# Performance work log

Measured on AMD Instinct MI355X. Metric: run time of the kernel, lower is better.

## Reference

```python
import jax, jax.numpy as jnp
import numpy as np

D_MODEL, N_HEADS, D_C, D_COMP, D_ROPE = 2048, 16, 512, 768, 64
D_HEAD = D_MODEL // N_HEADS  # 128
B, S = 2, 2048
ROPE_THETA = 10000.0


def _rope_cos_sin(seq_len, dim):
    # frequencies for pairwise complex rotation, dim = per-head rope dim (even)
    inv_freq = 1.0 / (ROPE_THETA ** (jnp.arange(0, dim, 2, dtype=jnp.float32) / dim))
    t = jnp.arange(seq_len, dtype=jnp.float32)
    ang = t[:, None] * inv_freq[None, :]  # [S, dim/2]
    return jnp.cos(ang), jnp.sin(ang)


def _apply_rope(x, cos, sin):
    # x: [B, S, H, dr]; rotate consecutive pairs (view_as_complex semantics)
    x1, x2 = x[..., 0::2], x[..., 1::2]
    c = cos[None, :, None, :]
    s = sin[None, :, None, :]
    y1 = x1 * c - x2 * s
    y2 = x1 * s + x2 * c
    return jnp.stack([y1, y2], axis=-1).reshape(x.shape)


def setup_inputs() -> dict:
    key = jax.random.key(0)
    ks = jax.random.split(key, 9)
    sc = 0.02
    return {
        "x": jax.random.normal(ks[0], (B, S, D_MODEL), jnp.float32),
        "Wd": jax.random.normal(ks[1], (D_MODEL, D_C), jnp.float32) * sc,
        "bd": jnp.zeros((D_C,), jnp.float32),
        "Wu": jax.random.normal(ks[2], (D_C, N_HEADS * D_HEAD), jnp.float32) * sc,
        "bu": jnp.zeros((N_HEADS * D_HEAD,), jnp.float32),
        "Wqd": jax.random.normal(ks[3], (D_MODEL, D_COMP), jnp.float32) * sc,
        "bqd": jnp.zeros((D_COMP,), jnp.float32),
        "Wqu": jax.random.normal(ks[4], (D_COMP, N_HEADS * D_HEAD), jnp.float32) * sc,
        "bqu": jnp.zeros((N_HEADS * D_HEAD,), jnp.float32),
        "Wqr": jax.random.normal(ks[5], (D_COMP, N_HEADS * D_ROPE), jnp.float32) * sc,
        "bqr": jnp.zeros((N_HEADS * D_ROPE,), jnp.float32),
        "Wkr": jax.random.normal(ks[6], (D_MODEL, N_HEADS * D_ROPE), jnp.float32) * sc,
        "bkr": jnp.zeros((N_HEADS * D_ROPE,), jnp.float32),
        "Wo": jax.random.normal(ks[7], (N_HEADS * D_HEAD, D_MODEL), jnp.float32) * sc,
        "bo": jnp.zeros((D_MODEL,), jnp.float32),
    }


def reference(x, Wd, bd, Wu, bu, Wqd, bqd, Wqu, bqu, Wqr, bqr, Wkr, bkr, Wo, bo):
    b, s, _ = x.shape
    # low-rank KV compression
    kv_c = x @ Wd + bd                                   # [B,S,d_c]
    kv_up = (kv_c @ Wu + bu).reshape(b, s, N_HEADS, D_HEAD)  # shared K-content / V
    # low-rank Q compression
    q_cmp = x @ Wqd + bqd                                # [B,S,d_comp]
    q_c = (q_cmp @ Wqu + bqu).reshape(b, s, N_HEADS, D_HEAD)
    # decoupled RoPE branches
    cos, sin = _rope_cos_sin(s, D_ROPE)
    q_r = _apply_rope((q_cmp @ Wqr + bqr).reshape(b, s, N_HEADS, D_ROPE), cos, sin)
    k_r = _apply_rope((x @ Wkr + bkr).reshape(b, s, N_HEADS, D_ROPE), cos, sin)
    q = jnp.concatenate([q_c, q_r], axis=-1)             # [B,S,H,dh+dr]
    k = jnp.concatenate([kv_up, k_r], axis=-1)           # [B,S,H,dh+dr]
    scale = 1.0 / np.sqrt(D_HEAD).astype(np.float32)
    scores = jnp.einsum('bqhd,bkhd->bhqk', q, k) * scale  # [B,H,S,S]
    probs = jax.nn.softmax(scores, axis=-1)
    out = jnp.einsum('bhqk,bkhd->bqhd', probs, kv_up)    # v == kv_up (as in source)
    out = out.reshape(b, s, N_HEADS * D_HEAD)
    return out @ Wo + bo
```

## Files before the change

kernel.cpp:

```cpp
#include <hip/hip_runtime.h>
#include <cmath>

typedef __bf16 bf16;
typedef __bf16 bf16x8 __attribute__((ext_vector_type(8)));
typedef __bf16 bf16x4 __attribute__((ext_vector_type(4)));
typedef __bf16 bf16x2 __attribute__((ext_vector_type(2)));
typedef float f32x4 __attribute__((ext_vector_type(4)));
typedef int i32x4 __attribute__((ext_vector_type(4)));

#define S_LEN 2048
#define QK_LD 3072

__device__ __forceinline__ void async_copy16(const bf16* g, bf16* l) {
    __builtin_amdgcn_global_load_lds(
        (const __attribute__((address_space(1))) void*)g,
        (__attribute__((address_space(3))) void*)l, 16, 0, 0);
}

__device__ __forceinline__ unsigned packbf(float a, float b) {
    bf16x2 v; v[0] = (bf16)a; v[1] = (bf16)b;
    return __builtin_bit_cast(unsigned, v);
}

__global__ __launch_bounds__(256) void cast_f32_bf16(const float* __restrict__ in,
                                                     bf16* __restrict__ out) {
    size_t i = ((size_t)blockIdx.x * 256 + threadIdx.x) * 8;
    float4 a = *(const float4*)(in + i);
    float4 b = *(const float4*)(in + i + 4);
    bf16x8 v;
    v[0] = (bf16)a.x; v[1] = (bf16)a.y; v[2] = (bf16)a.z; v[3] = (bf16)a.w;
    v[4] = (bf16)b.x; v[5] = (bf16)b.y; v[6] = (bf16)b.z; v[7] = (bf16)b.w;
    *(bf16x8*)(out + i) = v;
}

struct TSeg { const float* src; bf16* dst; int K, N, blk0; };
struct TArgs { TSeg s[7]; };

__global__ __launch_bounds__(256) void transpose_all(TArgs a) {
    __shared__ float tile[64][68];
    int b = blockIdx.x, si = 0;
#pragma unroll
    for (int i = 1; i < 7; ++i) if (b >= a.s[i].blk0) si = i;
    TSeg sg = a.s[si];
    int local = b - sg.blk0;
    int kTiles = sg.K >> 6;
    int kt = local % kTiles, nt = local / kTiles;
    int k0 = kt * 64, n0 = nt * 64;
    int K = sg.K, N = sg.N;
    int t = threadIdx.x;
#pragma unroll
    for (int i = 0; i < 4; ++i) {
        int c = t + i * 256;
        int r = c >> 4, off = (c & 15) * 4;
        float4 v = *(const float4*)(sg.src + (size_t)(k0 + r) * N + n0 + off);
        tile[r][off] = v.x; tile[r][off + 1] = v.y;
        tile[r][off + 2] = v.z; tile[r][off + 3] = v.w;
    }
    __syncthreads();
#pragma unroll
    for (int i = 0; i < 2; ++i) {
        int c = t + i * 256;
        int nr = c >> 3, koff = (c & 7) * 8;
        bf16x8 v;
#pragma unroll
        for (int j = 0; j < 8; ++j) v[j] = (bf16)tile[koff + j][nr];
        *(bf16x8*)(sg.dst + (size_t)(n0 + nr) * K + k0 + koff) = v;
    }
}

__global__ __launch_bounds__(256) void setup_small(const float* __restrict__ bd,
                                                   const float* __restrict__ bqd,
                                                   const float* __restrict__ bkr,
                                                   const float* __restrict__ bqu,
                                                   const float* __restrict__ bqr,
                                                   float* __restrict__ bcat,
                                                   float2* __restrict__ tab) {
    if (blockIdx.x < 21) {
        int i = blockIdx.x * 256 + threadIdx.x;
        if (i < 512) bcat[i] = bd[i];
        else if (i < 1280) bcat[i] = bqd[i - 512];
        else if (i < 2304) bcat[i] = bkr[i - 1280];
        else if (i < 4352) bcat[i] = bqu[i - 2304];
        else if (i < 5376) bcat[i] = bqr[i - 4352];
    } else {
        int id = (blockIdx.x - 21) * 256 + threadIdx.x;
        int s = id >> 5, i = id & 31;
        float f = expf(-0.2878231366242557f * (float)i);
        float ang = (float)s * f;
        tab[id] = make_float2(cosf(ang), sinf(ang));
    }
}

__device__ __forceinline__ void gemm_core(const bf16* __restrict__ A, int lda,
                                          const bf16* __restrict__ Bt,
                                          const float* __restrict__ bias,
                                          void* __restrict__ out0,
                                          void* __restrict__ out1,
                                          int Ndim, int Kdim, int mode,
                                          const float2* __restrict__ tab,
                                          int bn, int bm, bf16* As, bf16* Bs) {
    int t = threadIdx.x;
    int w = t >> 6, lane = t & 63;
    int wm = (w >> 1) * 64, wn = (w & 1) * 64;
    int l15 = lane & 15, q4 = lane >> 4;
    f32x4 acc[4][4] = {};

    int lrow = lane >> 2;
    int lcol = (lane & 3) * 8;
    int c0 = w * 2, c1 = w * 2 + 1;
    const bf16* aS0 = A  + (size_t)(bm * 128 + c0 * 16 + lrow) * lda + lcol;
    const bf16* aS1 = A  + (size_t)(bm * 128 + c1 * 16 + lrow) * lda + lcol;
    const bf16* bS0 = Bt + (size_t)(bn * 128 + c0 * 16 + lrow) * Kdim + lcol;
    const bf16* bS1 = Bt + (size_t)(bn * 128 + c1 * 16 + lrow) * Kdim + lcol;
    bf16* aD0 = &As[c0 * 512]; bf16* aD1 = &As[c1 * 512];
    bf16* bD0 = &Bs[c0 * 512]; bf16* bD1 = &Bs[c1 * 512];

    for (int kt = 0; kt < Kdim; kt += 32) {
        async_copy16(aS0 + kt, aD0);
        async_copy16(aS1 + kt, aD1);
        async_copy16(bS0 + kt, bD0);
        async_copy16(bS1 + kt, bD1);
        __syncthreads();
        bf16x8 af[4], bfr[4];
#pragma unroll
        for (int mb = 0; mb < 4; ++mb)
            af[mb] = *(const bf16x8*)&As[(wm + mb * 16 + l15) * 32 + q4 * 8];
#pragma unroll
        for (int nb = 0; nb < 4; ++nb)
            bfr[nb] = *(const bf16x8*)&Bs[(wn + nb * 16 + l15) * 32 + q4 * 8];
#pragma unroll
        for (int mb = 0; mb < 4; ++mb)
#pragma unroll
            for (int nb = 0; nb < 4; ++nb)
                acc[mb][nb] = __builtin_amdgcn_mfma_f32_16x16x32_bf16(
                    af[mb], bfr[nb], acc[mb][nb], 0, 0, 0);
        __syncthreads();
    }

#pragma unroll
    for (int mb = 0; mb < 4; ++mb) {
        int row = bm * 128 + wm + mb * 16 + q4 * 4;
#pragma unroll
        for (int nb = 0; nb < 4; ++nb) {
            int col = bn * 128 + wn + nb * 16 + l15;
            float bv = bias[col];
            if (mode == 1) {
#pragma unroll
                for (int r = 0; r < 4; ++r)
                    ((float*)out0)[(size_t)(row + r) * Ndim + col] = acc[mb][nb][r] + bv;
            } else if (mode == 4) {
                if (col < 1280) {
#pragma unroll
                    for (int r = 0; r < 4; ++r)
                        ((bf16*)out0)[(size_t)(row + r) * 2304 + col] =
                            (bf16)(acc[mb][nb][r] + bv);
                } else {
                    int rel = col - 1280;
                    int hh = rel >> 6, idx = rel & 63, ii = idx >> 1, odd = idx & 1;
#pragma unroll
                    for (int r = 0; r < 4; ++r) {
                        float vv = acc[mb][nb][r] + bv;
                        float pp = __shfl_xor(vv, 1, 64);
                        float2 cs = tab[((row + r) & 2047) * 32 + ii];
                        float o = vv * cs.x + (odd ? pp * cs.y : -pp * cs.y);
                        ((bf16*)out1)[(size_t)(row + r) * QK_LD + hh * 192 + 128 + idx] =
                            (bf16)o;
                    }
                }
            } else if (mode == 5) {
                if (col < 2048) {
                    int hh = col >> 7, dd = col & 127;
#pragma unroll
                    for (int r = 0; r < 4; ++r)
                        ((bf16*)out0)[(size_t)(row + r) * QK_LD + hh * 192 + dd] =
                            (bf16)(acc[mb][nb][r] + bv);
                } else {
                    int rel = col - 2048;
                    int hh = rel >> 6, idx = rel & 63, ii = idx >> 1, odd = idx & 1;
#pragma unroll
                    for (int r = 0; r < 4; ++r) {
                        float vv = acc[mb][nb][r] + bv;
                        float pp = __shfl_xor(vv, 1, 64);
                        float2 cs = tab[((row + r) & 2047) * 32 + ii];
                        float o = vv * cs.x + (odd ? pp * cs.y : -pp * cs.y);
                        ((bf16*)out0)[(size_t)(row + r) * QK_LD + hh * 192 + 128 + idx] =
                            (bf16)o;
                    }
                }
            } else {
                int hh = col >> 7, dd = col & 127;
                bf16x4 pack;
#pragma unroll
                for (int r = 0; r < 4; ++r) {
                    float vv = acc[mb][nb][r] + bv;
                    ((bf16*)out0)[(size_t)(row + r) * QK_LD + hh * 192 + dd] = (bf16)vv;
                    pack[r] = (bf16)vv;
                }
                int bidx = row >> 11, srow = row & 2047;
                *(bf16x4*)((bf16*)out1 +
                           ((size_t)(bidx * 16 + hh) * 128 + dd) * S_LEN + srow) = pack;
            }
        }
    }
}

__global__ __launch_bounds__(256) void gemm_bt(const bf16* __restrict__ A, int lda,
                                               const bf16* __restrict__ Bt,
                                               const float* __restrict__ bias,
                                               void* __restrict__ out0,
                                               void* __restrict__ out1,
                                               int Ndim, int Kdim, int mode,
                                               const float2* __restrict__ tab) {
    __shared__ bf16 As[128 * 32];
    __shared__ bf16 Bs[128 * 32];
    gemm_core(A, lda, Bt, bias, out0, out1, Ndim, Kdim, mode, tab,
              blockIdx.x, blockIdx.y, As, Bs);
}

__global__ __launch_bounds__(256) void gemm_up(const bf16* __restrict__ xproj,
                                               const bf16* __restrict__ WuT,
                                               const float* __restrict__ bu,
                                               void* __restrict__ kbuf,
                                               void* __restrict__ vt,
                                               const bf16* __restrict__ W2T,
                                               const float* __restrict__ bq,
                                               void* __restrict__ qbuf,
                                               const float2* __restrict__ tab) {
    __shared__ bf16 As[128 * 32];
    __shared__ bf16 Bs[128 * 32];
    int bn = blockIdx.x;
    if (bn < 16)
        gemm_core(xproj, 2304, WuT, bu, kbuf, vt, 2048, 512, 6, tab,
                  bn, blockIdx.y, As, Bs);
    else
        gemm_core(xproj + 512, 2304, W2T, bq, qbuf, nullptr, 3072, 768, 5, tab,
                  bn - 16, blockIdx.y, As, Bs);
}

__global__ __launch_bounds__(512, 4) void attn(const bf16* __restrict__ qbuf,
                                               const bf16* __restrict__ kbuf,
                                               const bf16* __restrict__ vt,
                                               bf16* __restrict__ attnout) {
    __shared__ bf16 Ks[2][32 * 192];
    __shared__ bf16 Vs[2][128 * 32];
    int bh = blockIdx.x;
    int qt = blockIdx.y;
    int b = bh >> 4, h = bh & 15;
    int t = threadIdx.x, w = t >> 6, lane = t & 63;
    int l15 = lane & 15, q4 = lane >> 4;
    const float scale = 0.08838834764831845f;

    bf16x8 qf[6];
    {
        size_t base = (size_t)(b * S_LEN + qt * 128 + w * 16 + l15) * QK_LD + h * 192;
#pragma unroll
        for (int c = 0; c < 6; ++c)
            qf[c] = *(const bf16x8*)(qbuf + base + c * 32 + q4 * 8);
    }

    f32x4 oacc[8] = {};
    float denom = 0.f;
    const bf16* kb_base = kbuf + (size_t)b * S_LEN * QK_LD + h * 192;
    const bf16* vt_base = vt + (size_t)bh * 128 * S_LEN;

    int kg0, kl0, kg1, kl1, vg0, vl0;
    {
        int c = t;
        int kr = c / 24, u = c % 24;
        kg0 = kr * QK_LD + u * 8;
        kl0 = kr * 192 + ((u ^ (kr & 7)) << 3);
    }
    {
        int c = t + 512;
        int kr = c / 24, u = c % 24;
        kg1 = kr * QK_LD + u * 8;
        kl1 = kr * 192 + ((u ^ (kr & 7)) << 3);
    }
    {
        int c = t;
        int vd = c >> 2, u = c & 3;
        vg0 = vd * S_LEN + u * 8;
        vl0 = vd * 32 + ((u ^ (vd & 3)) << 3);
    }
    bool kx = (t < 256);

    int srcA = ((lane & 16) << 1) + l15;
    int srcB = srcA + 16;
    bool hiK = lane >= 32;

    i32x4 kreg0, kreg1, vreg0;
    kreg0 = *(const i32x4*)(kb_base + kg0);
    if (kx) kreg1 = *(const i32x4*)(kb_base + kg1);
    vreg0 = *(const i32x4*)(vt_base + vg0);
    *(i32x4*)&Ks[0][kl0] = kreg0;
    if (kx) *(i32x4*)&Ks[0][kl1] = kreg1;
    *(i32x4*)&Vs[0][vl0] = vreg0;
    __syncthreads();

    int cur = 0;
    for (int kt = 0; kt < 64; ++kt) {
        if (kt < 63) {
            const bf16* kb = kb_base + (size_t)(kt + 1) * 32 * QK_LD;
            kreg0 = *(const i32x4*)(kb + kg0);
            if (kx) kreg1 = *(const i32x4*)(kb + kg1);
            vreg0 = *(const i32x4*)(vt_base + (kt + 1) * 32 + vg0);
        }

        f32x4 sacc[2] = {};
        __builtin_amdgcn_s_setprio(1);
#pragma unroll
        for (int c = 0; c < 6; ++c) {
#pragma unroll
            for (int nk = 0; nk < 2; ++nk) {
                bf16x8 kb = *(const bf16x8*)&Ks[cur][(nk * 16 + l15) * 192 +
                              (((c * 4 + q4) ^ (l15 & 7)) << 3)];
                sacc[nk] = __builtin_amdgcn_mfma_f32_16x16x32_bf16(
                    kb, qf[c], sacc[nk], 0, 0, 0);
            }
        }
        __builtin_amdgcn_s_setprio(0);

        unsigned pk[2][2];
#pragma unroll
        for (int nk = 0; nk < 2; ++nk) {
            float e[4];
#pragma unroll
            for (int r = 0; r < 4; ++r) {
                e[r] = __expf(fminf(sacc[nk][r] * scale, 50.0f));
                denom += e[r];
            }
            pk[nk][0] = packbf(e[0], e[1]);
            pk[nk][1] = packbf(e[2], e[3]);
        }
        bf16x8 paf;
        {
            unsigned d[4];
#pragma unroll
            for (int p = 0; p < 4; ++p) {
                int sl = (p & 2) ? srcB : srcA;
                unsigned va = (unsigned)__shfl((int)pk[0][p & 1], sl, 64);
                unsigned vb = (unsigned)__shfl((int)pk[1][p & 1], sl, 64);
                d[p] = hiK ? vb : va;
            }
            i32x4 di;
            di[0] = (int)d[0]; di[1] = (int)d[1];
            di[2] = (int)d[2]; di[3] = (int)d[3];
            paf = __builtin_bit_cast(bf16x8, di);
        }

        __builtin_amdgcn_s_setprio(1);
#pragma unroll
        for (int nb = 0; nb < 8; ++nb) {
            bf16x8 vb = *(const bf16x8*)&Vs[cur][(nb * 16 + l15) * 32 +
                          ((q4 ^ (l15 & 3)) << 3)];
            oacc[nb] = __builtin_amdgcn_mfma_f32_16x16x32_bf16(
                paf, vb, oacc[nb], 0, 0, 0);
        }
        __builtin_amdgcn_s_setprio(0);

        if (kt < 63) {
            *(i32x4*)&Ks[cur ^ 1][kl0] = kreg0;
            if (kx) *(i32x4*)&Ks[cur ^ 1][kl1] = kreg1;
            *(i32x4*)&Vs[cur ^ 1][vl0] = vreg0;
        }
        __syncthreads();
        cur ^= 1;
    }

    denom += __shfl_xor(denom, 16, 64);
    denom += __shfl_xor(denom, 32, 64);

#pragma unroll
    for (int r = 0; r < 4; ++r) {
        float dv = __shfl(denom, q4 * 4 + r, 64);
        float inv = 1.0f / dv;
        int row = qt * 128 + w * 16 + q4 * 4 + r;
#pragma unroll
        for (int nb = 0; nb < 8; ++nb) {
            int col = h * 128 + nb * 16 + l15;
            attnout[(size_t)(b * S_LEN + row) * 2048 + col] =
                (bf16)(oacc[nb][r] * inv);
        }
    }
}

extern "C" void kernel_launch(void* const* d_in, const int* in_sizes, int n_in,
                              void* d_out, int out_size, void* d_ws, size_t ws_size,
                              hipStream_t stream) {
    const float* x   = (const float*)d_in[0];
    const float* Wd  = (const float*)d_in[1];
    const float* bd  = (const float*)d_in[2];
    const float* Wu  = (const float*)d_in[3];
    const float* bu  = (const float*)d_in[4];
    const float* Wqd = (const float*)d_in[5];
    const float* bqd = (const float*)d_in[6];
    const float* Wqu = (const float*)d_in[7];
    const float* bqu = (const float*)d_in[8];
    const float* Wqr = (const float*)d_in[9];
    const float* bqr = (const float*)d_in[10];
    const float* Wkr = (const float*)d_in[11];
    const float* bkr = (const float*)d_in[12];
    const float* Wo  = (const float*)d_in[13];
    const float* bo  = (const float*)d_in[14];
    float* out = (float*)d_out;

    char* p = (char*)d_ws;
    auto alloc = [&](size_t n) { char* r = p; p += (n + 255) & ~(size_t)255; return r; };
    bf16* xb    = (bf16*)alloc((size_t)4096 * 2048 * 2);
    bf16* W1T   = (bf16*)alloc((size_t)2304 * 2048 * 2);
    bf16* W2T   = (bf16*)alloc((size_t)3072 * 768 * 2);
    bf16* WuT   = (bf16*)alloc((size_t)2048 * 512 * 2);
    bf16* WoT   = (bf16*)alloc((size_t)2048 * 2048 * 2);
    bf16* xproj = (bf16*)alloc((size_t)4096 * 2304 * 2);
    bf16* qbuf  = (bf16*)alloc((size_t)4096 * 3072 * 2);
    bf16* kbuf  = (bf16*)alloc((size_t)4096 * 3072 * 2);
    bf16* vt    = (bf16*)alloc((size_t)32 * 128 * 2048 * 2);
    bf16* aout  = (bf16*)alloc((size_t)4096 * 2048 * 2);
    float* bcat = (float*)alloc((size_t)5376 * 4);
    float2* tab = (float2*)alloc((size_t)65536 * 8);

    cast_f32_bf16<<<dim3(4096), dim3(256), 0, stream>>>(x, xb);

    TArgs ta;
    ta.s[0] = {Wd,  W1T,                       2048, 512,  0};
    ta.s[1] = {Wqd, W1T + (size_t)512 * 2048,  2048, 768,  256};
    ta.s[2] = {Wkr, W1T + (size_t)1280 * 2048, 2048, 1024, 640};
    ta.s[3] = {Wqu, W2T,                       768,  2048, 1152};
    ta.s[4] = {Wqr, W2T + (size_t)2048 * 768,  768,  1024, 1536};
    ta.s[5] = {Wu,  WuT,                       512,  2048, 1728};
    ta.s[6] = {Wo,  WoT,                       2048, 2048, 1984};
    transpose_all<<<dim3(3008), dim3(256), 0, stream>>>(ta);
    setup_small<<<dim3(277), dim3(256), 0, stream>>>(bd, bqd, bkr, bqu, bqr, bcat, tab);

    gemm_bt<<<dim3(18, 32), dim3(256), 0, stream>>>(xb, 2048, W1T, bcat,
                                                    xproj, kbuf, 2304, 2048, 4, tab);
    gemm_up<<<dim3(40, 32), dim3(256), 0, stream>>>(xproj, WuT, bu, kbuf, vt,
                                                    W2T, bcat + 2304, qbuf, tab);

    attn<<<dim3(32, 16), dim3(512), 0, stream>>>(qbuf, kbuf, vt, aout);

    gemm_bt<<<dim3(16, 32), dim3(256), 0, stream>>>(aout, 2048, WoT, bo,
                                                    out, nullptr, 2048, 2048, 1, tab);
}
```

Baseline: 439.4 us.

## Switch attention to 32x32x16 MFMA tiles with 32 query rows per wave

The attention kernel now uses 32x32x16 bf16 MFMA instead of 16x16x32, so each wave handles 32 query rows and each block 256 rows; the grid is halved to match. The K/V shared-memory layout and XOR swizzle are rewritten around 8-byte chunks to fit the new operand fragment shapes. The P fragment is rebuilt with a single xor-32 shuffle. The aim is to reuse each K/V LDS read across more query rows and cut instruction count, at the cost of more registers (launch bounds lowered to 2) and fewer blocks, which risks lower occupancy and poorer load balance.

```diff
diff --git a/kernel.cpp b/kernel.cpp
--- a/kernel.cpp
+++ b/kernel.cpp
@@ -6,7 +6,9 @@
 typedef __bf16 bf16x4 __attribute__((ext_vector_type(4)));
 typedef __bf16 bf16x2 __attribute__((ext_vector_type(2)));
 typedef float f32x4 __attribute__((ext_vector_type(4)));
+typedef float f32x16 __attribute__((ext_vector_type(16)));
 typedef int i32x4 __attribute__((ext_vector_type(4)));
+typedef int i32x2 __attribute__((ext_vector_type(2)));
 
 #define S_LEN 2048
 #define QK_LD 3072
@@ -237,7 +239,7 @@
                   bn - 16, blockIdx.y, As, Bs);
 }
 
-__global__ __launch_bounds__(512, 4) void attn(const bf16* __restrict__ qbuf,
+__global__ __launch_bounds__(512, 2) void attn(const bf16* __restrict__ qbuf,
                                                const bf16* __restrict__ kbuf,
                                                const bf16* __restrict__ vt,
                                                bf16* __restrict__ attnout) {
@@ -247,54 +249,76 @@
     int qt = blockIdx.y;
     int b = bh >> 4, h = bh & 15;
     int t = threadIdx.x, w = t >> 6, lane = t & 63;
-    int l15 = lane & 15, q4 = lane >> 4;
+    int l31 = lane & 31, hl = lane >> 5;
     const float scale = 0.08838834764831845f;
 
-    bf16x8 qf[6];
+    bf16x8 qf[12];
     {
-        size_t base = (size_t)(b * S_LEN + qt * 128 + w * 16 + l15) * QK_LD + h * 192;
-#pragma unroll
-        for (int c = 0; c < 6; ++c)
-            qf[c] = *(const bf16x8*)(qbuf + base + c * 32 + q4 * 8);
-    }
-
-    f32x4 oacc[8] = {};
+        size_t rbase = (size_t)(b * S_LEN + qt * 256 + w * 32 + l31) * QK_LD
+                       + h * 192 + hl * 8;
+#pragma unroll
+        for (int c = 0; c < 12; ++c)
+            qf[c] = *(const bf16x8*)(qbuf + rbase + c * 16);
+    }
+
+    f32x16 oacc[4] = {};
     float denom = 0.f;
     const bf16* kb_base = kbuf + (size_t)b * S_LEN * QK_LD + h * 192;
     const bf16* vt_base = vt + (size_t)bh * 128 * S_LEN;
 
-    int kg0, kl0, kg1, kl1, vg0, vl0;
+    int kg0, klA0, klB0, kg1, klA1, klB1, vg0, vlA0, vlB0;
     {
         int c = t;
         int kr = c / 24, u = c % 24;
         kg0 = kr * QK_LD + u * 8;
-        kl0 = kr * 192 + ((u ^ (kr & 7)) << 3);
+        int m = kr & 15;
+        klA0 = kr * 192 + (((2 * u) ^ m) << 2);
+        klB0 = kr * 192 + (((2 * u + 1) ^ m) << 2);
     }
     {
         int c = t + 512;
         int kr = c / 24, u = c % 24;
         kg1 = kr * QK_LD + u * 8;
-        kl1 = kr * 192 + ((u ^ (kr & 7)) << 3);
+        int m = kr & 15;
+        klA1 = kr * 192 + (((2 * u) ^ m) << 2);
+        klB1 = kr * 192 + (((2 * u + 1) ^ m) << 2);
     }
     {
         int c = t;
         int vd = c >> 2, u = c & 3;
         vg0 = vd * S_LEN + u * 8;
-        vl0 = vd * 32 + ((u ^ (vd & 3)) << 3);
+        int line = vd >> 1, lm = line & 15;
+        int sl = 8 * (vd & 1) + 2 * u;
+        vlA0 = line * 64 + ((sl ^ lm) << 2);
+        vlB0 = line * 64 + (((sl + 1) ^ lm) << 2);
     }
     bool kx = (t < 256);
 
-    int srcA = ((lane & 16) << 1) + l15;
-    int srcB = srcA + 16;
-    bool hiK = lane >= 32;
+    int mK = l31 & 15;
+    int kRow = l31 * 192;
+    int vLM = l31 >> 1;
+    int vSlotB = 8 * (l31 & 1) + 2 * hl;
 
     i32x4 kreg0, kreg1, vreg0;
     kreg0 = *(const i32x4*)(kb_base + kg0);
     if (kx) kreg1 = *(const i32x4*)(kb_base + kg1);
     vreg0 = *(const i32x4*)(vt_base + vg0);
-    *(i32x4*)&Ks[0][kl0] = kreg0;
-    if (kx) *(i32x4*)&Ks[0][kl1] = kreg1;
-    *(i32x4*)&Vs[0][vl0] = vreg0;
+    {
+        i32x2 lo; lo[0] = kreg0[0]; lo[1] = kreg0[1];
+        i32x2 hi; hi[0] = kreg0[2]; hi[1] = kreg0[3];
+        *(i32x2*)&Ks[0][klA0] = lo;
+        *(i32x2*)&Ks[0][klB0] = hi;
+        if (kx) {
+            i32x2 lo1; lo1[0] = kreg1[0]; lo1[1] = kreg1[1];
+            i32x2 hi1; hi1[0] = kreg1[2]; hi1[1] = kreg1[3];
+            *(i32x2*)&Ks[0][klA1] = lo1;
+            *(i32x2*)&Ks[0][klB1] = hi1;
+        }
+        i32x2 lov; lov[0] = vreg0[0]; lov[1] = vreg0[1];
+        i32x2 hiv; hiv[0] = vreg0[2]; hiv[1] = vreg0[3];
+        *(i32x2*)&Vs[0][vlA0] = lov;
+        *(i32x2*)&Vs[0][vlB0] = hiv;
+    }
     __syncthreads();
 
     int cur = 0;
@@ -306,80 +330,92 @@
             vreg0 = *(const i32x4*)(vt_base + (kt + 1) * 32 + vg0);
         }
 
-        f32x4 sacc[2] = {};
+        f32x16 sacc = {};
         __builtin_amdgcn_s_setprio(1);
 #pragma unroll
-        for (int c = 0; c < 6; ++c) {
-#pragma unroll
-            for (int nk = 0; nk < 2; ++nk) {
-                bf16x8 kb = *(const bf16x8*)&Ks[cur][(nk * 16 + l15) * 192 +
-                              (((c * 4 + q4) ^ (l15 & 7)) << 3)];
-                sacc[nk] = __builtin_amdgcn_mfma_f32_16x16x32_bf16(
-                    kb, qf[c], sacc[nk], 0, 0, 0);
+        for (int c = 0; c < 12; ++c) {
+            int u0 = 4 * c + 2 * hl;
+            i32x2 lo = *(const i32x2*)&Ks[cur][kRow + ((u0 ^ mK) << 2)];
+            i32x2 hi = *(const i32x2*)&Ks[cur][kRow + (((u0 + 1) ^ mK) << 2)];
+            i32x4 kv; kv[0] = lo[0]; kv[1] = lo[1]; kv[2] = hi[0]; kv[3] = hi[1];
+            bf16x8 kb = __builtin_bit_cast(bf16x8, kv);
+            sacc = __builtin_amdgcn_mfma_f32_32x32x16_bf16(kb, qf[c], sacc, 0, 0, 0);
+        }
+        __builtin_amdgcn_s_setprio(0);
+
+        unsigned W[8], pw[8];
+#pragma unroll
+        for (int m = 0; m < 8; ++m) {
+            float e0 = __expf(fminf(sacc[2 * m] * scale, 50.0f));
+            float e1 = __expf(fminf(sacc[2 * m + 1] * scale, 50.0f));
+            denom += e0 + e1;
+            W[m] = packbf(e0, e1);
+        }
+#pragma unroll
+        for (int m = 0; m < 8; ++m)
+            pw[m] = (unsigned)__shfl_xor((int)W[m], 32, 64);
+        bf16x8 paf[2];
+#pragma unroll
+        for (int s = 0; s < 2; ++s) {
+            unsigned A = hl ? pw[4 * s + 2] : W[4 * s + 0];
+            unsigned B = hl ? pw[4 * s + 3] : W[4 * s + 1];
+            unsigned C = hl ? W[4 * s + 2] : pw[4 * s + 0];
+            unsigned D = hl ? W[4 * s + 3] : pw[4 * s + 1];
+            i32x4 di; di[0] = (int)A; di[1] = (int)B; di[2] = (int)C; di[3] = (int)D;
+            paf[s] = __builtin_bit_cast(bf16x8, di);
+        }
+
+        __builtin_amdgcn_s_setprio(1);
+#pragma unroll
+        for (int dg = 0; dg < 4; ++dg) {
+#pragma unroll
+            for (int s = 0; s < 2; ++s) {
+                int line = dg * 16 + (l31 >> 1);
+                int s0 = (vSlotB + 4 * s) ^ vLM;
+                int s1 = (vSlotB + 4 * s + 1) ^ vLM;
+                i32x2 lo = *(const i32x2*)&Vs[cur][line * 64 + (s0 << 2)];
+                i32x2 hi = *(const i32x2*)&Vs[cur][line * 64 + (s1 << 2)];
+                i32x4 vv; vv[0] = lo[0]; vv[1] = lo[1]; vv[2] = hi[0]; vv[3] = hi[1];
+                bf16x8 vb = __builtin_bit_cast(bf16x8, vv);
+                oacc[dg] = __builtin_amdgcn_mfma_f32_32x32x16_bf16(
+                    paf[s], vb, oacc[dg], 0, 0, 0);
             }
         }
         __builtin_amdgcn_s_setprio(0);
 
-        unsigned pk[2][2];
-#pragma unroll
-        for (int nk = 0; nk < 2; ++nk) {
-            float e[4];
-#pragma unroll
-            for (int r = 0; r < 4; ++r) {
-                e[r] = __expf(fminf(sacc[nk][r] * scale, 50.0f));
-                denom += e[r];
+        if (kt < 63) {
+            i32x2 lo; lo[0] = kreg0[0]; lo[1] = kreg0[1];
+            i32x2 hi; hi[0] = kreg0[2]; hi[1] = kreg0[3];
+            *(i32x2*)&Ks[cur ^ 1][klA0] = lo;
+            *(i32x2*)&Ks[cur ^ 1][klB0] = hi;
+            if (kx) {
+                i32x2 lo1; lo1[0] = kreg1[0]; lo1[1] = kreg1[1];
+                i32x2 hi1; hi1[0] = kreg1[2]; hi1[1] = kreg1[3];
+                *(i32x2*)&Ks[cur ^ 1][klA1] = lo1;
+                *(i32x2*)&Ks[cur ^ 1][klB1] = hi1;
             }
-            pk[nk][0] = packbf(e[0], e[1]);
-            pk[nk][1] = packbf(e[2], e[3]);
-        }
-        bf16x8 paf;
-        {
-            unsigned d[4];
-#pragma unroll
-            for (int p = 0; p < 4; ++p) {
-                int sl = (p & 2) ? srcB : srcA;
-                unsigned va = (unsigned)__shfl((int)pk[0][p & 1], sl, 64);
-                unsigned vb = (unsigned)__shfl((int)pk[1][p & 1], sl, 64);
-                d[p] = hiK ? vb : va;
-            }
-            i32x4 di;
-            di[0] = (int)d[0]; di[1] = (int)d[1];
-            di[2] = (int)d[2]; di[3] = (int)d[3];
-            paf = __builtin_bit_cast(bf16x8, di);
-        }
-
-        __builtin_amdgcn_s_setprio(1);
-#pragma unroll
-        for (int nb = 0; nb < 8; ++nb) {
-            bf16x8 vb = *(const bf16x8*)&Vs[cur][(nb * 16 + l15) * 32 +
-                          ((q4 ^ (l15 & 3)) << 3)];
-            oacc[nb] = __builtin_amdgcn_mfma_f32_16x16x32_bf16(
-                paf, vb, oacc[nb], 0, 0, 0);
-        }
-        __builtin_amdgcn_s_setprio(0);
-
-        if (kt < 63) {
-            *(i32x4*)&Ks[cur ^ 1][kl0] = kreg0;
-            if (kx) *(i32x4*)&Ks[cur ^ 1][kl1] = kreg1;
-            *(i32x4*)&Vs[cur ^ 1][vl0] = vreg0;
+            i32x2 lov; lov[0] = vreg0[0]; lov[1] = vreg0[1];
+            i32x2 hiv; hiv[0] = vreg0[2]; hiv[1] = vreg0[3];
+            *(i32x2*)&Vs[cur ^ 1][vlA0] = lov;
+            *(i32x2*)&Vs[cur ^ 1][vlB0] = hiv;
         }
         __syncthreads();
         cur ^= 1;
     }
 
-    denom += __shfl_xor(denom, 16, 64);
     denom += __shfl_xor(denom, 32, 64);
 
 #pragma unroll
-    for (int r = 0; r < 4; ++r) {
-        float dv = __shfl(denom, q4 * 4 + r, 64);
+    for (int r = 0; r < 16; ++r) {
+        int rowl = (r & 3) + 8 * (r >> 2) + 4 * hl;
+        float dv = __shfl(denom, rowl, 64);
         float inv = 1.0f / dv;
-        int row = qt * 128 + w * 16 + q4 * 4 + r;
-#pragma unroll
-        for (int nb = 0; nb < 8; ++nb) {
-            int col = h * 128 + nb * 16 + l15;
+        int row = qt * 256 + w * 32 + rowl;
+#pragma unroll
+        for (int dg = 0; dg < 4; ++dg) {
+            int col = h * 128 + dg * 32 + l31;
             attnout[(size_t)(b * S_LEN + row) * 2048 + col] =
-                (bf16)(oacc[nb][r] * inv);
+                (bf16)(oacc[dg][r] * inv);
         }
     }
 }
@@ -437,7 +473,7 @@
     gemm_up<<<dim3(40, 32), dim3(256), 0, stream>>>(xproj, WuT, bu, kbuf, vt,
                                                     W2T, bcat + 2304, qbuf, tab);
 
-    attn<<<dim3(32, 16), dim3(512), 0, stream>>>(qbuf, kbuf, vt, aout);
+    attn<<<dim3(32, 8), dim3(512), 0, stream>>>(qbuf, kbuf, vt, aout);
 
     gemm_bt<<<dim3(16, 32), dim3(256), 0, stream>>>(aout, 2048, WoT, bo,
                                                     out, nullptr, 2048, 2048, 1, tab);
```

Result: faster. 430.2 us (-2.1%).
